# Optimization experiments

Hardware: AMD Instinct MI355X
Metric: run time of the kernel (lower is better)

The kernel has to match this reference:

```python
import jax, jax.numpy as jnp
import numpy as np

N_NODES = 50000
N_EDGES = 1000000
C = 32          # nchannels (multiplicity of each irrep)
NBESSEL = 8
WEIGHT_NUMEL = 3 * C  # three uvu paths: 0e->0e, 0e->1o, 0e->2e


def setup_inputs() -> dict:
    key = jax.random.key(0)
    ks = jax.random.split(key, 12)
    inp = {
        "lenght": jax.random.uniform(ks[0], (N_EDGES, NBESSEL), dtype=jnp.float32),
        "node_features": jax.random.normal(ks[1], (N_NODES, C), dtype=jnp.float32),
        "edge_attributes": jax.random.normal(ks[2], (N_EDGES, 9), dtype=jnp.float32),
        "edge_index": jax.random.randint(ks[3], (2, N_EDGES), 0, N_NODES, dtype=jnp.int64),
        # FullyConnectedNet([8, 6, 6, 6, 96]) weights (e3nn stores unnormalized W, divides by sqrt(fan_in))
        "fcn_w0": jax.random.normal(ks[4], (NBESSEL, 6), dtype=jnp.float32),
        "fcn_w1": jax.random.normal(ks[5], (6, 6), dtype=jnp.float32),
        "fcn_w2": jax.random.normal(ks[6], (6, 6), dtype=jnp.float32),
        "fcn_w3": jax.random.normal(ks[7], (6, WEIGHT_NUMEL), dtype=jnp.float32),
        # equivariant Linear irreps_mid -> irreps_out: one [C, C] mixing matrix per l in {0,1,2}
        "lin_w0": jax.random.normal(ks[8], (C, C), dtype=jnp.float32),
        "lin_w1": jax.random.normal(ks[9], (C, C), dtype=jnp.float32),
        "lin_w2": jax.random.normal(ks[10], (C, C), dtype=jnp.float32),
    }
    return inp


def _fcn(x, w0, w1, w2, w3):
    # e3nn FullyConnectedNet: normalized linear layers with SiLU on hidden layers
    for w in (w0, w1, w2):
        x = jax.nn.silu((x @ w) * (1.0 / np.float32(np.sqrt(w.shape[0]))))
    return (x @ w3) * (1.0 / np.float32(np.sqrt(w3.shape[0])))


def reference(lenght, node_features, edge_attributes, edge_index,
              fcn_w0, fcn_w1, fcn_w2, fcn_w3, lin_w0, lin_w1, lin_w2):
    sender = edge_index[0]
    receiver = edge_index[1]
    num_nodes = node_features.shape[0]
    c = node_features.shape[1]
    e = lenght.shape[0]

    # per-edge tensor-product weights: [E, 3C]
    tp_w = _fcn(lenght, fcn_w0, fcn_w1, fcn_w2, fcn_w3)
    w0, w1, w2 = tp_w[:, :c], tp_w[:, c:2 * c], tp_w[:, 2 * c:]

    x = node_features[sender]                       # gather: [E, C]
    y0 = edge_attributes[:, 0:1]                    # 0e: [E, 1]
    y1 = edge_attributes[:, 1:4]                    # 1o: [E, 3]
    y2 = edge_attributes[:, 4:9]                    # 2e: [E, 5]

    # uvu tensor product, CG for 0e x l -> l is identity
    m0 = w0 * x * y0                                # [E, C]
    m1 = (w1 * x)[:, :, None] * y1[:, None, :]      # [E, C, 3]
    m2 = (w2 * x)[:, :, None] * y2[:, None, :]      # [E, C, 5]
    mij = jnp.concatenate(
        [m0, m1.reshape(e, 3 * c), m2.reshape(e, 5 * c)], axis=1)  # [E, 9C]

    # scatter_sum over receivers
    msg = jax.ops.segment_sum(mij, receiver, num_segments=num_nodes)  # [N, 9C]

    # equivariant Linear (per-l channel mixing, 1/sqrt(fan_in) normalization)
    inv = 1.0 / np.float32(np.sqrt(c))
    o0 = (msg[:, :c] @ lin_w0) * inv                                   # [N, C]
    o1 = jnp.einsum('nci,cd->ndi', msg[:, c:4 * c].reshape(num_nodes, c, 3), lin_w1) * inv
    o2 = jnp.einsum('nci,cd->ndi', msg[:, 4 * c:].reshape(num_nodes, c, 5), lin_w2) * inv
    return jnp.concatenate(
        [o0, o1.reshape(num_nodes, 3 * c), o2.reshape(num_nodes, 5 * c)], axis=1)
```

## Files before the change

### kernel.cpp

```cpp
#include <hip/hip_runtime.h>
#include <math.h>

#define N_NODES 50000
#define N_EDGES 1000000
#define CCH     32
#define ROW     288
#define SCAN_BLOCKS 196

__global__ __launch_bounds__(256) void hist_kernel(
    const int* __restrict__ edge_index, int* __restrict__ deg)
{
    const int e = blockIdx.x * 256 + threadIdx.x;
    if (e >= N_EDGES) return;
    atomicAdd(&deg[edge_index[N_EDGES + e]], 1);
}

__global__ __launch_bounds__(256) void scan_local_kernel(
    const int* __restrict__ deg, int* __restrict__ lexcl, int* __restrict__ blocksum)
{
    __shared__ int s[256];
    const int t = threadIdx.x;
    const int gid = blockIdx.x * 256 + t;
    const int v = (gid < N_NODES) ? deg[gid] : 0;
    s[t] = v;
    __syncthreads();
    for (int ofs = 1; ofs < 256; ofs <<= 1) {
        int w = (t >= ofs) ? s[t - ofs] : 0;
        __syncthreads();
        s[t] += w;
        __syncthreads();
    }
    if (gid < N_NODES) lexcl[gid] = s[t] - v;
    if (t == 255) blocksum[blockIdx.x] = s[255];
}

__global__ __launch_bounds__(256) void scan_top_kernel(
    const int* __restrict__ blocksum, int* __restrict__ blockpref)
{
    __shared__ int s[256];
    const int t = threadIdx.x;
    const int v = (t < SCAN_BLOCKS) ? blocksum[t] : 0;
    s[t] = v;
    __syncthreads();
    for (int ofs = 1; ofs < 256; ofs <<= 1) {
        int w = (t >= ofs) ? s[t - ofs] : 0;
        __syncthreads();
        s[t] += w;
        __syncthreads();
    }
    if (t < SCAN_BLOCKS) blockpref[t] = s[t] - v;
}

__global__ __launch_bounds__(256) void scan_addback_kernel(
    const int* __restrict__ lexcl, const int* __restrict__ blockpref,
    int* __restrict__ offset, int* __restrict__ cursor)
{
    const int gid = blockIdx.x * 256 + threadIdx.x;
    if (gid >= N_NODES) return;
    const int base = blockpref[blockIdx.x] + lexcl[gid];
    offset[gid] = base;
    cursor[gid] = base;
}

__global__ __launch_bounds__(256) void pack_kernel(
    const float* __restrict__ lenght,
    const float* __restrict__ edge_attr,
    const int*   __restrict__ edge_index,
    const float* __restrict__ fw0,
    const float* __restrict__ fw1,
    const float* __restrict__ fw2,
    int*         __restrict__ cursor,
    float4*      __restrict__ rec,
    int2*        __restrict__ es)
{
    __shared__ float s_w[120];
    for (int i = threadIdx.x; i < 120; i += 256)
        s_w[i] = (i < 48) ? fw0[i] : (i < 84) ? fw1[i - 48] : fw2[i - 84];
    __syncthreads();
    const float* sw0 = s_w;
    const float* sw1 = s_w + 48;
    const float* sw2 = s_w + 84;

    const int e = blockIdx.x * 256 + threadIdx.x;
    if (e >= N_EDGES) return;

    const float inv8 = 0.35355339059327373f;
    const float inv6 = 0.4082482904638631f;

    float len[8];
    const float4 l0 = ((const float4*)(lenght + (long long)e * 8))[0];
    const float4 l1 = ((const float4*)(lenght + (long long)e * 8))[1];
    len[0]=l0.x; len[1]=l0.y; len[2]=l0.z; len[3]=l0.w;
    len[4]=l1.x; len[5]=l1.y; len[6]=l1.z; len[7]=l1.w;

    float h0[6], h1[6], h2[6];
    #pragma unroll
    for (int j = 0; j < 6; ++j) {
        float a = 0.f;
        #pragma unroll
        for (int k = 0; k < 8; ++k) a += len[k] * sw0[k * 6 + j];
        a *= inv8;
        h0[j] = a / (1.f + __expf(-a));
    }
    #pragma unroll
    for (int j = 0; j < 6; ++j) {
        float a = 0.f;
        #pragma unroll
        for (int k = 0; k < 6; ++k) a += h0[k] * sw1[k * 6 + j];
        a *= inv6;
        h1[j] = a / (1.f + __expf(-a));
    }
    #pragma unroll
    for (int j = 0; j < 6; ++j) {
        float a = 0.f;
        #pragma unroll
        for (int k = 0; k < 6; ++k) a += h1[k] * sw2[k * 6 + j];
        a *= inv6;
        h2[j] = a * inv6 / (1.f + __expf(-a));
    }

    const float* ea = edge_attr + (long long)e * 9;
    float y[9];
    #pragma unroll
    for (int i = 0; i < 9; ++i) y[i] = ea[i];

    const int snd = edge_index[e];
    const int r   = edge_index[N_EDGES + e];
    const int p   = atomicAdd(&cursor[r], 1);
    es[p] = make_int2(e, snd);

    float4* rp = rec + (long long)e * 4;
    rp[0] = make_float4(h2[0], h2[1], h2[2], h2[3]);
    rp[1] = make_float4(h2[4], h2[5], y[0], y[1]);
    rp[2] = make_float4(y[2], y[3], y[4], y[5]);
    rp[3] = make_float4(y[6], y[7], y[8], __int_as_float(snd));
}

__global__ __launch_bounds__(256) void gather_kernel(
    const float4* __restrict__ rec,
    const float*  __restrict__ node_features,
    const int2*   __restrict__ es,
    const int*    __restrict__ offset,
    const int*    __restrict__ deg,
    const float*  __restrict__ fw3,
    const float*  __restrict__ lw0,
    const float*  __restrict__ lw1,
    const float*  __restrict__ lw2,
    float*        __restrict__ out)
{
    __shared__ float s_lw0[1024], s_lw1[1024], s_lw2[1024];
    for (int i = threadIdx.x; i < 1024; i += 256) {
        s_lw0[i] = lw0[i];
        s_lw1[i] = lw1[i];
        s_lw2[i] = lw2[i];
    }
    __syncthreads();

    const int wave = threadIdx.x >> 6;
    const int l    = threadIdx.x & 63;
    const int c    = l & 31;
    const int h    = l >> 5;
    const int node = blockIdx.x * 4 + wave;

    float f3a[6], f3b[6], f3c[6];
    #pragma unroll
    for (int k = 0; k < 6; ++k) {
        f3a[k] = fw3[k * 96 + c];
        f3b[k] = fw3[k * 96 + 32 + c];
        f3c[k] = fw3[k * 96 + 64 + c];
    }

    const int off = offset[node];
    const int dg  = deg[node];

    float acc[9] = {0.f,0.f,0.f,0.f,0.f,0.f,0.f,0.f,0.f};

    if (dg > h) {
        const int2* esp = es + off;
        const int last = dg - 1;

        int2 eA = esp[min(h,     last)];
        int2 eB = esp[min(h + 2, last)];
        const float4* pa = rec + (long long)eA.x * 4;
        float4 A0 = pa[0], A1 = pa[1], A2 = pa[2], A3 = pa[3];
        float  xA = node_features[(long long)eA.y * CCH + c];
        const float4* pb = rec + (long long)eB.x * 4;
        float4 B0 = pb[0], B1 = pb[1], B2 = pb[2], B3 = pb[3];
        float  xB = node_features[(long long)eB.y * CCH + c];
        eA = esp[min(h + 4, last)];
        eB = esp[min(h + 6, last)];

        int j = h;
        while (true) {
            {
                const int eid = eA.x, snd = eA.y;
                eA = esp[min(j + 8, last)];
                const float w0c = A0.x*f3a[0] + A0.y*f3a[1] + A0.z*f3a[2]
                                + A0.w*f3a[3] + A1.x*f3a[4] + A1.y*f3a[5];
                const float w1c = A0.x*f3b[0] + A0.y*f3b[1] + A0.z*f3b[2]
                                + A0.w*f3b[3] + A1.x*f3b[4] + A1.y*f3b[5];
                const float w2c = A0.x*f3c[0] + A0.y*f3c[1] + A0.z*f3c[2]
                                + A0.w*f3c[3] + A1.x*f3c[4] + A1.y*f3c[5];
                const float x = xA;
                acc[0] += (w0c * x) * A1.z;
                const float a1 = w1c * x;
                acc[1] += a1 * A1.w;
                acc[2] += a1 * A2.x;
                acc[3] += a1 * A2.y;
                const float a2 = w2c * x;
                acc[4] += a2 * A2.z;
                acc[5] += a2 * A2.w;
                acc[6] += a2 * A3.x;
                acc[7] += a2 * A3.y;
                acc[8] += a2 * A3.z;
                const float4* rp = rec + (long long)eid * 4;
                A0 = rp[0]; A1 = rp[1]; A2 = rp[2]; A3 = rp[3];
                xA = node_features[(long long)snd * CCH + c];
            }
            j += 2;
            if (j >= dg) break;
            {
                const int eid = eB.x, snd = eB.y;
                eB = esp[min(j + 8, last)];
                const float w0c = B0.x*f3a[0] + B0.y*f3a[1] + B0.z*f3a[2]
                                + B0.w*f3a[3] + B1.x*f3a[4] + B1.y*f3a[5];
                const float w1c = B0.x*f3b[0] + B0.y*f3b[1] + B0.z*f3b[2]
                                + B0.w*f3b[3] + B1.x*f3b[4] + B1.y*f3b[5];
                const float w2c = B0.x*f3c[0] + B0.y*f3c[1] + B0.z*f3c[2]
                                + B0.w*f3c[3] + B1.x*f3c[4] + B1.y*f3c[5];
                const float x = xB;
                acc[0] += (w0c * x) * B1.z;
                const float a1 = w1c * x;
                acc[1] += a1 * B1.w;
                acc[2] += a1 * B2.x;
                acc[3] += a1 * B2.y;
                const float a2 = w2c * x;
                acc[4] += a2 * B2.z;
                acc[5] += a2 * B2.w;
                acc[6] += a2 * B3.x;
                acc[7] += a2 * B3.y;
                acc[8] += a2 * B3.z;
                const float4* rp = rec + (long long)eid * 4;
                B0 = rp[0]; B1 = rp[1]; B2 = rp[2]; B3 = rp[3];
                xB = node_features[(long long)snd * CCH + c];
            }
            j += 2;
            if (j >= dg) break;
        }
    }

    #pragma unroll
    for (int k = 0; k < 9; ++k) acc[k] += __shfl_down(acc[k], 32);

    const int d = c;
    float o0 = 0.f;
    float o1[3] = {0.f, 0.f, 0.f};
    float o2[5] = {0.f, 0.f, 0.f, 0.f, 0.f};
    for (int cc = h * 16; cc < h * 16 + 16; ++cc) {
        const float m0 = __shfl(acc[0], cc);
        const float m1 = __shfl(acc[1], cc);
        const float m2 = __shfl(acc[2], cc);
        const float m3 = __shfl(acc[3], cc);
        const float m4 = __shfl(acc[4], cc);
        const float m5 = __shfl(acc[5], cc);
        const float m6 = __shfl(acc[6], cc);
        const float m7 = __shfl(acc[7], cc);
        const float m8 = __shfl(acc[8], cc);
        o0 += m0 * s_lw0[cc * 32 + d];
        const float w1 = s_lw1[cc * 32 + d];
        o1[0] += m1 * w1; o1[1] += m2 * w1; o1[2] += m3 * w1;
        const float w2 = s_lw2[cc * 32 + d];
        o2[0] += m4 * w2; o2[1] += m5 * w2; o2[2] += m6 * w2;
        o2[3] += m7 * w2; o2[4] += m8 * w2;
    }

    o0 += __shfl_down(o0, 32);
    #pragma unroll
    for (int i = 0; i < 3; ++i) o1[i] += __shfl_down(o1[i], 32);
    #pragma unroll
    for (int i = 0; i < 5; ++i) o2[i] += __shfl_down(o2[i], 32);

    if (h == 0) {
        const float inv32 = 0.17677669529663687f;
        float* op = out + (long long)node * ROW;
        op[d] = o0 * inv32;
        #pragma unroll
        for (int i = 0; i < 3; ++i) op[32 + d * 3 + i] = o1[i] * inv32;
        #pragma unroll
        for (int i = 0; i < 5; ++i) op[128 + d * 5 + i] = o2[i] * inv32;
    }
}

extern "C" void kernel_launch(void* const* d_in, const int* in_sizes, int n_in,
                              void* d_out, int out_size, void* d_ws, size_t ws_size,
                              hipStream_t stream)
{
    const float* lenght = (const float*)d_in[0];
    const float* nf     = (const float*)d_in[1];
    const float* ea     = (const float*)d_in[2];
    const int*   ei     = (const int*)d_in[3];
    const float* fw0    = (const float*)d_in[4];
    const float* fw1    = (const float*)d_in[5];
    const float* fw2    = (const float*)d_in[6];
    const float* fw3    = (const float*)d_in[7];
    const float* lw0    = (const float*)d_in[8];
    const float* lw1    = (const float*)d_in[9];
    const float* lw2    = (const float*)d_in[10];
    float* out = (float*)d_out;

    char* ws = (char*)d_ws;
    float4* rec    = (float4*)ws; ws += (size_t)N_EDGES * 4 * sizeof(float4);
    int2* es       = (int2*)ws;   ws += (size_t)N_EDGES * sizeof(int2);
    int* deg       = (int*)ws;    ws += (size_t)N_NODES * sizeof(int);
    int* offset    = (int*)ws;    ws += (size_t)N_NODES * sizeof(int);
    int* cursor    = (int*)ws;    ws += (size_t)N_NODES * sizeof(int);
    int* lexcl     = (int*)ws;    ws += (size_t)N_NODES * sizeof(int);
    int* blocksum  = (int*)ws;    ws += (size_t)SCAN_BLOCKS * sizeof(int);
    int* blockpref = (int*)ws;    ws += (size_t)SCAN_BLOCKS * sizeof(int);

    hipMemsetAsync(deg, 0, (size_t)N_NODES * sizeof(int), stream);

    const int EB = (N_EDGES + 255) / 256;
    hist_kernel        <<<EB, 256, 0, stream>>>(ei, deg);
    scan_local_kernel  <<<SCAN_BLOCKS, 256, 0, stream>>>(deg, lexcl, blocksum);
    scan_top_kernel    <<<1, 256, 0, stream>>>(blocksum, blockpref);
    scan_addback_kernel<<<SCAN_BLOCKS, 256, 0, stream>>>(lexcl, blockpref, offset, cursor);
    pack_kernel        <<<EB, 256, 0, stream>>>(lenght, ea, ei, fw0, fw1, fw2, cursor, rec, es);
    gather_kernel      <<<N_NODES / 4, 256, 0, stream>>>(
        rec, nf, es, offset, deg, fw3, lw0, lw1, lw2, out);
}
```

Baseline: 403.0 us.

## Scatter per-edge records into receiver-sorted order during pack

The pack kernel now writes each edge's 64-byte record at its CSR slot instead of at its original edge index. The edge-slot array shrinks to just sender ids. The gather kernel then reads records contiguously per node rather than through an indirect random gather, which removes one dependent load and makes the record reads sequential. In exchange the pack kernel's record stores become scattered writes, and the prefetch now reads records by slot index.

```diff
diff --git a/kernel.cpp b/kernel.cpp
--- a/kernel.cpp
+++ b/kernel.cpp
@@ -71,7 +71,7 @@
     const float* __restrict__ fw2,
     int*         __restrict__ cursor,
     float4*      __restrict__ rec,
-    int2*        __restrict__ es)
+    int*         __restrict__ esnd)
 {
     __shared__ float s_w[120];
     for (int i = threadIdx.x; i < 120; i += 256)
@@ -127,9 +127,10 @@
     const int snd = edge_index[e];
     const int r   = edge_index[N_EDGES + e];
     const int p   = atomicAdd(&cursor[r], 1);
-    es[p] = make_int2(e, snd);
-
-    float4* rp = rec + (long long)e * 4;
+
+    esnd[p] = snd;
+
+    float4* rp = rec + (long long)p * 4;
     rp[0] = make_float4(h2[0], h2[1], h2[2], h2[3]);
     rp[1] = make_float4(h2[4], h2[5], y[0], y[1]);
     rp[2] = make_float4(y[2], y[3], y[4], y[5]);
@@ -139,7 +140,7 @@
 __global__ __launch_bounds__(256) void gather_kernel(
     const float4* __restrict__ rec,
     const float*  __restrict__ node_features,
-    const int2*   __restrict__ es,
+    const int*    __restrict__ esnd,
     const int*    __restrict__ offset,
     const int*    __restrict__ deg,
     const float*  __restrict__ fw3,
@@ -176,25 +177,30 @@
     float acc[9] = {0.f,0.f,0.f,0.f,0.f,0.f,0.f,0.f,0.f};
 
     if (dg > h) {
-        const int2* esp = es + off;
         const int last = dg - 1;
-
-        int2 eA = esp[min(h,     last)];
-        int2 eB = esp[min(h + 2, last)];
-        const float4* pa = rec + (long long)eA.x * 4;
+        const float4* rbase = rec + (long long)off * 4;
+        const int*    sbase = esnd + off;
+
+        int sA = sbase[min(h,     last)];
+        int sB = sbase[min(h + 2, last)];
+        const float4* pa = rbase + (long long)min(h,     last) * 4;
+        const float4* pb = rbase + (long long)min(h + 2, last) * 4;
         float4 A0 = pa[0], A1 = pa[1], A2 = pa[2], A3 = pa[3];
-        float  xA = node_features[(long long)eA.y * CCH + c];
-        const float4* pb = rec + (long long)eB.x * 4;
         float4 B0 = pb[0], B1 = pb[1], B2 = pb[2], B3 = pb[3];
-        float  xB = node_features[(long long)eB.y * CCH + c];
-        eA = esp[min(h + 4, last)];
-        eB = esp[min(h + 6, last)];
+        float  xA = node_features[(long long)sA * CCH + c];
+        float  xB = node_features[(long long)sB * CCH + c];
+        sA = sbase[min(h + 4, last)];
+        sB = sbase[min(h + 6, last)];
 
         int j = h;
         while (true) {
             {
-                const int eid = eA.x, snd = eA.y;
-                eA = esp[min(j + 8, last)];
+                const int sn = sA;
+                sA = sbase[min(j + 8, last)];
+                const float4* rp = rbase + (long long)min(j + 4, last) * 4;
+                const float4 n0 = rp[0], n1 = rp[1], n2 = rp[2], n3 = rp[3];
+                const float  xn = node_features[(long long)sn * CCH + c];
+
                 const float w0c = A0.x*f3a[0] + A0.y*f3a[1] + A0.z*f3a[2]
                                 + A0.w*f3a[3] + A1.x*f3a[4] + A1.y*f3a[5];
                 const float w1c = A0.x*f3b[0] + A0.y*f3b[1] + A0.z*f3b[2]
@@ -213,15 +219,18 @@
                 acc[6] += a2 * A3.x;
                 acc[7] += a2 * A3.y;
                 acc[8] += a2 * A3.z;
-                const float4* rp = rec + (long long)eid * 4;
-                A0 = rp[0]; A1 = rp[1]; A2 = rp[2]; A3 = rp[3];
-                xA = node_features[(long long)snd * CCH + c];
+
+                A0 = n0; A1 = n1; A2 = n2; A3 = n3; xA = xn;
             }
             j += 2;
             if (j >= dg) break;
             {
-                const int eid = eB.x, snd = eB.y;
-                eB = esp[min(j + 8, last)];
+                const int sn = sB;
+                sB = sbase[min(j + 8, last)];
+                const float4* rp = rbase + (long long)min(j + 4, last) * 4;
+                const float4 n0 = rp[0], n1 = rp[1], n2 = rp[2], n3 = rp[3];
+                const float  xn = node_features[(long long)sn * CCH + c];
+
                 const float w0c = B0.x*f3a[0] + B0.y*f3a[1] + B0.z*f3a[2]
                                 + B0.w*f3a[3] + B1.x*f3a[4] + B1.y*f3a[5];
                 const float w1c = B0.x*f3b[0] + B0.y*f3b[1] + B0.z*f3b[2]
@@ -240,9 +249,8 @@
                 acc[6] += a2 * B3.x;
                 acc[7] += a2 * B3.y;
                 acc[8] += a2 * B3.z;
-                const float4* rp = rec + (long long)eid * 4;
-                B0 = rp[0]; B1 = rp[1]; B2 = rp[2]; B3 = rp[3];
-                xB = node_features[(long long)snd * CCH + c];
+
+                B0 = n0; B1 = n1; B2 = n2; B3 = n3; xB = xn;
             }
             j += 2;
             if (j >= dg) break;
@@ -310,7 +318,7 @@
 
     char* ws = (char*)d_ws;
     float4* rec    = (float4*)ws; ws += (size_t)N_EDGES * 4 * sizeof(float4);
-    int2* es       = (int2*)ws;   ws += (size_t)N_EDGES * sizeof(int2);
+    int* esnd      = (int*)ws;    ws += (size_t)N_EDGES * sizeof(int);
     int* deg       = (int*)ws;    ws += (size_t)N_NODES * sizeof(int);
     int* offset    = (int*)ws;    ws += (size_t)N_NODES * sizeof(int);
     int* cursor    = (int*)ws;    ws += (size_t)N_NODES * sizeof(int);
@@ -325,7 +333,7 @@
     scan_local_kernel  <<<SCAN_BLOCKS, 256, 0, stream>>>(deg, lexcl, blocksum);
     scan_top_kernel    <<<1, 256, 0, stream>>>(blocksum, blockpref);
     scan_addback_kernel<<<SCAN_BLOCKS, 256, 0, stream>>>(lexcl, blockpref, offset, cursor);
-    pack_kernel        <<<EB, 256, 0, stream>>>(lenght, ea, ei, fw0, fw1, fw2, cursor, rec, es);
+    pack_kernel        <<<EB, 256, 0, stream>>>(lenght, ea, ei, fw0, fw1, fw2, cursor, rec, esnd);
     gather_kernel      <<<N_NODES / 4, 256, 0, stream>>>(
-        rec, nf, es, offset, deg, fw3, lw0, lw1, lw2, out);
-}
+        rec, nf, esnd, offset, deg, fw3, lw0, lw1, lw2, out);
+}
```

After: 410.0 us. About the same (+1.7%).
